# Kernel optimization log

Hardware: AMD Instinct MI355X
Metric: run time of the kernel (lower is better)

Reference implementation:

```python
import jax, jax.numpy as jnp
import numpy as np

B, S, D, F, TOPK = 8, 2048, 1024, 64, 8


def setup_inputs() -> dict:
    key = jax.random.key(0)
    ks = jax.random.split(key, 4)
    scale = 1.0 / np.sqrt(D)
    return {
        "x": jax.random.normal(ks[0], (B, S, D), dtype=jnp.float32),
        "W_top": jax.random.normal(ks[1], (D, F), dtype=jnp.float32) * scale,
        "b_top": jnp.zeros((F,), dtype=jnp.float32),
        "W_feat": jax.random.normal(ks[2], (D, F), dtype=jnp.float32) * scale,
        "b_feat": jnp.zeros((F,), dtype=jnp.float32),
        "W_gates": jax.random.normal(ks[3], (F, D), dtype=jnp.float32) * scale,
        "b_gates": jnp.zeros((F,), dtype=jnp.float32),
        "alpha": jnp.ones((1,), dtype=jnp.float32),
        "num": TOPK,
    }


def reference(x, W_top, b_top, W_feat, b_feat, W_gates, b_gates, alpha, num):
    # Router logits and top-k selection: [B,S,F] -> vals/idx [B,S,num]
    top_logits = jnp.einsum("bsd,df->bsf", x, W_top) + b_top
    vals, idx = jax.lax.top_k(top_logits, num)
    sm = jax.nn.softmax(vals, axis=-1)                     # softmax over selected experts
    # Scatter softmax'd top-k weights into dense [B,S,F] (zeros elsewhere)
    onehot = jax.nn.one_hot(idx, F, dtype=sm.dtype)        # [B,S,num,F]
    type_dense = jnp.einsum("bsk,bskf->bsf", sm, onehot)
    # Dense softmax routing branch
    feat_soft = jax.nn.softmax(jnp.einsum("bsd,df->bsf", x, W_feat) + b_feat, axis=-1)
    a = jax.nn.sigmoid(alpha)                              # [1], broadcasts
    features = a * type_dense + (1.0 - a) * feat_soft      # [B,S,F]
    # num_feature small Linear(dims,1)+Sigmoid gates fused into one GEMM
    gates = jax.nn.sigmoid(jnp.einsum("bsd,fd->bsf", x, W_gates) + b_gates)  # [B,S,F]
    # Weighted sum over feature axis; original returns shape [B,S,1]
    return jnp.sum(gates * features, axis=-1, keepdims=True)
```

## Files before the change

kernel.cpp:

```cpp
#include <hip/hip_runtime.h>
#include <hip/hip_bf16.h>
#include <math.h>

#define D_DIM 1024
#define TOKB  32
#define NCH   32

typedef short  bf16x8 __attribute__((ext_vector_type(8)));
typedef float  f32x4  __attribute__((ext_vector_type(4)));

__device__ __forceinline__ ushort f2bf(float f) {
  uint u = __float_as_uint(f);
  return (ushort)((u + 0x7fffu + ((u >> 16) & 1u)) >> 16);
}
__device__ __forceinline__ float bf2f(ushort h) {
  return __uint_as_float(((uint)h) << 16);
}
__device__ __forceinline__ float sigm(float v) {
  return 1.f / (1.f + expf(-v));
}
__device__ __forceinline__ void conv8(const f32x4 va, const f32x4 vb,
                                      bf16x8& ah, bf16x8& al) {
  uint* AH = reinterpret_cast<uint*>(&ah);
  uint* AL = reinterpret_cast<uint*>(&al);
#pragma unroll
  for (int p = 0; p < 4; ++p) {
    float a = (p < 2) ? va[2 * p]     : vb[2 * (p - 2)];
    float b = (p < 2) ? va[2 * p + 1] : vb[2 * (p - 2) + 1];
    __hip_bfloat162 h2 = __float22bfloat162_rn(float2{a, b});
    uint hu;
    __builtin_memcpy(&hu, &h2, 4);
    AH[p] = hu;
    float ra = a - __uint_as_float(hu << 16);
    float rb = b - __uint_as_float(hu & 0xffff0000u);
    __hip_bfloat162 l2 = __float22bfloat162_rn(float2{ra, rb});
    uint lu;
    __builtin_memcpy(&lu, &l2, 4);
    AL[p] = lu;
  }
}

__global__ __launch_bounds__(256) void pack_w_kernel(
    const float* __restrict__ Wt, const float* __restrict__ Wf,
    const float* __restrict__ Wg, ushort* __restrict__ Wp) {
  int gid = blockIdx.x * 256 + threadIdx.x;
  if (gid >= 32 * 12 * 64 * 4) return;
  int jp   = gid & 3;
  int t    = gid >> 2;
  int lane = t & 63;
  int t2   = t >> 6;
  int fb   = t2 % 12;
  int ks   = t2 / 12;
  int k0   = ks * 32 + ((lane >> 4) << 3) + jp * 2;
  int f    = fb * 16 + (lane & 15);
  float v0, v1;
  if (f < 64)       { v0 = Wt[k0 * 64 + f];            v1 = Wt[(k0 + 1) * 64 + f]; }
  else if (f < 128) { v0 = Wf[k0 * 64 + f - 64];       v1 = Wf[(k0 + 1) * 64 + f - 64]; }
  else              { v0 = Wg[(f - 128) * D_DIM + k0]; v1 = Wg[(f - 128) * D_DIM + k0 + 1]; }
  ushort h0 = f2bf(v0), h1 = f2bf(v1);
  ushort l0 = f2bf(v0 - bf2f(h0)), l1 = f2bf(v1 - bf2f(h1));
  size_t base = ((size_t)(ks * 12 + fb) * 2) * 512 + lane * 8 + jp * 2;
  *(uint*)(Wp + base)       = (uint)h0 | ((uint)h1 << 16);
  *(uint*)(Wp + base + 512) = (uint)l0 | ((uint)l1 << 16);
}

__global__ __launch_bounds__(512, 4) void moe_gate_kernel(
    const float* __restrict__ x, const ushort* __restrict__ Wp,
    const float* __restrict__ b_top, const float* __restrict__ b_feat,
    const float* __restrict__ b_gates, const float* __restrict__ alpha,
    const int* __restrict__ nump, float* __restrict__ out) {
  __shared__ float L[32 * 196 + 192];
  float* bsm = L + 32 * 196;
  const int tid  = threadIdx.x;
  const int lane = tid & 63;
  const int wid  = tid >> 6;
  const int tg   = wid >> 2;
  const int wc   = wid & 3;
  const int tok0 = blockIdx.x * TOKB;

  if (tid < 192)
    bsm[tid] = (tid < 64) ? b_top[tid]
             : (tid < 128) ? b_feat[tid - 64] : b_gates[tid - 128];

  const float* xp = x + (size_t)(tok0 + tg * 16 + (lane & 15)) * D_DIM
                      + ((lane >> 4) << 3);
  const ushort* wbase = Wp + (size_t)(wc * 3) * 1024 + lane * 8;

  f32x4 acc[3] = {};
  bf16x8 bAh[3], bAl[3], bBh[3], bBl[3];
  f32x4 xA[2], xB[2];

#define LOADB(BH, BL, c) do {                                        \
    const ushort* wp_ = wbase + (size_t)(c) * 12288;                 \
    _Pragma("unroll")                                                \
    for (int q = 0; q < 3; ++q) {                                    \
      BH[q] = *(const bf16x8*)(wp_ + q * 1024);                      \
      BL[q] = *(const bf16x8*)(wp_ + q * 1024 + 512);                \
    } } while (0)
#define LOADX(XR, c) do {                                            \
    XR[0] = *(const f32x4*)(xp + (c) * 32);                          \
    XR[1] = *(const f32x4*)(xp + (c) * 32 + 4); } while (0)
#define COMPUTE(XR, BH, BL) do {                                     \
    bf16x8 ah, al;                                                   \
    conv8(XR[0], XR[1], ah, al);                                     \
    _Pragma("unroll")                                                \
    for (int q = 0; q < 3; ++q) {                                    \
      acc[q] = __builtin_amdgcn_mfma_f32_16x16x32_bf16(ah, BH[q], acc[q], 0, 0, 0); \
      acc[q] = __builtin_amdgcn_mfma_f32_16x16x32_bf16(al, BH[q], acc[q], 0, 0, 0); \
      acc[q] = __builtin_amdgcn_mfma_f32_16x16x32_bf16(ah, BL[q], acc[q], 0, 0, 0); \
    } } while (0)

  LOADB(bAh, bAl, 0);
  LOADX(xA, 0);
  for (int c = 0; c < NCH; c += 2) {
    LOADB(bBh, bBl, c + 1);
    LOADX(xB, c + 1);
    COMPUTE(xA, bAh, bAl);
    if (c + 2 < NCH) {
      LOADB(bAh, bAl, c + 2);
      LOADX(xA, c + 2);
    }
    COMPUTE(xB, bBh, bBl);
  }
#undef LOADB
#undef LOADX
#undef COMPUTE

  __syncthreads();
#pragma unroll
  for (int q = 0; q < 3; ++q) {
    int f = wc * 48 + q * 16 + (lane & 15);
    int t = tg * 16 + ((lane >> 4) << 2);
    float bv = bsm[f];
#pragma unroll
    for (int r = 0; r < 4; ++r)
      L[(t + r) * 196 + f] = acc[q][r] + bv;
  }
  __syncthreads();

  if (tid < 256) {
    const int t   = tid >> 3;
    const int sub = tid & 7;
    const float* Lr = L + t * 196;
    float tp[8], ftv[8], gtv[8];
#pragma unroll
    for (int j = 0; j < 8; ++j) {
      int f = sub + 8 * j;
      tp[j]  = Lr[f];
      ftv[j] = Lr[64 + f];
      gtv[j] = sigm(Lr[128 + f]);
    }
    float mf = ftv[0];
#pragma unroll
    for (int j = 1; j < 8; ++j) mf = fmaxf(mf, ftv[j]);
#pragma unroll
    for (int m = 1; m < 8; m <<= 1) mf = fmaxf(mf, __shfl_xor(mf, m, 8));
    float Zf = 0.f, Sf = 0.f;
#pragma unroll
    for (int j = 0; j < 8; ++j) {
      float e = expf(ftv[j] - mf);
      Zf += e;
      Sf = fmaf(gtv[j], e, Sf);
    }
#pragma unroll
    for (int m = 1; m < 8; m <<= 1) {
      Zf += __shfl_xor(Zf, m, 8);
      Sf += __shfl_xor(Sf, m, 8);
    }
    int num = *nump;
    num = num < 1 ? 1 : (num > 64 ? 64 : num);
    uint sel8 = 0;
    float m0 = 0.f, Zt = 0.f, St = 0.f;
    for (int k = 0; k < num; ++k) {
      float bv = -3.4e38f; int bj = -1;
#pragma unroll
      for (int j = 0; j < 8; ++j)
        if (!((sel8 >> j) & 1u) && tp[j] > bv) { bv = tp[j]; bj = j; }
      int bf = (bj >= 0) ? (sub + 8 * bj) : (1 << 30);
#pragma unroll
      for (int m = 1; m < 8; m <<= 1) {
        float ov = __shfl_xor(bv, m, 8);
        int   of = __shfl_xor(bf, m, 8);
        if (ov > bv || (ov == bv && of < bf)) { bv = ov; bf = of; }
      }
      if (k == 0) m0 = bv;
      float e = expf(bv - m0);
      Zt += e;
      St = fmaf(sigm(Lr[128 + bf]), e, St);
      if ((bf & 7) == sub) sel8 |= 1u << (bf >> 3);
    }
    if (sub == 0) {
      float a = sigm(alpha[0]);
      out[tok0 + t] = a * (St / Zt) + (1.f - a) * (Sf / Zf);
    }
  }
}

extern "C" void kernel_launch(void* const* d_in, const int* in_sizes, int n_in,
                              void* d_out, int out_size, void* d_ws, size_t ws_size,
                              hipStream_t stream) {
  const float* x       = (const float*)d_in[0];
  const float* W_top   = (const float*)d_in[1];
  const float* b_top   = (const float*)d_in[2];
  const float* W_feat  = (const float*)d_in[3];
  const float* b_feat  = (const float*)d_in[4];
  const float* W_gates = (const float*)d_in[5];
  const float* b_gates = (const float*)d_in[6];
  const float* alpha   = (const float*)d_in[7];
  const int*   nump    = (const int*)d_in[8];
  float*       out     = (float*)d_out;
  ushort*      Wp      = (ushort*)d_ws;

  int n_tok = in_sizes[0] / D_DIM;
  hipLaunchKernelGGL(pack_w_kernel, dim3(384), dim3(256), 0, stream,
                     W_top, W_feat, W_gates, Wp);
  hipLaunchKernelGGL(moe_gate_kernel, dim3(n_tok / TOKB), dim3(512), 0, stream,
                     x, Wp, b_top, b_feat, b_gates, alpha, nump, out);
}
```

Measured before the change: 162.7 us.

## Stage packed weights into LDS via async global_load_lds double buffering

Previously every wave loaded its own copy of the packed bf16 hi/lo weight fragments straight from global memory into registers, so all 8 waves in a block fetched redundant weight data. The new code has the waves cooperatively copy each 24 KB weight chunk into shared memory with global_load_lds. It double-buffers those chunks with explicit vmcnt waits and barriers while x is still read directly into registers. This cuts global/L2 weight traffic and register pressure, but adds a block-wide barrier per chunk and raises LDS use to about 49 KB, which may limit occupancy.

```diff
diff --git a/kernel.cpp b/kernel.cpp
--- a/kernel.cpp
+++ b/kernel.cpp
@@ -18,6 +18,10 @@
 }
 __device__ __forceinline__ float sigm(float v) {
   return 1.f / (1.f + expf(-v));
+}
+__device__ __forceinline__ void gload16(const void* g, void* l) {
+  __builtin_amdgcn_global_load_lds((const __attribute__((address_space(1))) void*)g,
+                                   (__attribute__((address_space(3))) void*)l, 16, 0, 0);
 }
 __device__ __forceinline__ void conv8(const f32x4 va, const f32x4 vb,
                                       bf16x8& ah, bf16x8& al) {
@@ -69,8 +73,12 @@
     const float* __restrict__ b_top, const float* __restrict__ b_feat,
     const float* __restrict__ b_gates, const float* __restrict__ alpha,
     const int* __restrict__ nump, float* __restrict__ out) {
-  __shared__ float L[32 * 196 + 192];
-  float* bsm = L + 32 * 196;
+  __shared__ __align__(16) char smem[49920];
+  char* buf0 = smem;
+  char* buf1 = smem + 24576;
+  float* bsm = (float*)(smem + 49152);
+  float* L   = (float*)smem;
+
   const int tid  = threadIdx.x;
   const int lane = tid & 63;
   const int wid  = tid >> 6;
@@ -84,47 +92,77 @@
 
   const float* xp = x + (size_t)(tok0 + tg * 16 + (lane & 15)) * D_DIM
                       + ((lane >> 4) << 3);
-  const ushort* wbase = Wp + (size_t)(wc * 3) * 1024 + lane * 8;
+  const int stgu = wid * 1024;
+  const char* wsrc = (const char*)Wp + stgu + lane * 16;
+  const int fro = wc * 6144 + lane * 16;
 
   f32x4 acc[3] = {};
-  bf16x8 bAh[3], bAl[3], bBh[3], bBl[3];
-  f32x4 xA[2], xB[2];
-
-#define LOADB(BH, BL, c) do {                                        \
-    const ushort* wp_ = wbase + (size_t)(c) * 12288;                 \
-    _Pragma("unroll")                                                \
-    for (int q = 0; q < 3; ++q) {                                    \
-      BH[q] = *(const bf16x8*)(wp_ + q * 1024);                      \
-      BL[q] = *(const bf16x8*)(wp_ + q * 1024 + 512);                \
-    } } while (0)
-#define LOADX(XR, c) do {                                            \
-    XR[0] = *(const f32x4*)(xp + (c) * 32);                          \
-    XR[1] = *(const f32x4*)(xp + (c) * 32 + 4); } while (0)
-#define COMPUTE(XR, BH, BL) do {                                     \
+  f32x4 xA0, xA1, xB0, xB1;
+
+#define STAGE(dbuf, c) do {                                          \
+    const char* s_ = wsrc + (size_t)(c) * 24576;                     \
+    char* d_ = (dbuf) + stgu;                                        \
+    gload16(s_, d_);                                                 \
+    gload16(s_ + 8192,  d_ + 8192);                                  \
+    gload16(s_ + 16384, d_ + 16384); } while (0)
+#define COMPUTE(cbuf, X0, X1) do {                                   \
+    const char* bp_ = (cbuf) + fro;                                  \
+    bf16x8 bh0 = *(const bf16x8*)(bp_);                              \
+    bf16x8 bl0 = *(const bf16x8*)(bp_ + 1024);                       \
+    bf16x8 bh1 = *(const bf16x8*)(bp_ + 2048);                       \
+    bf16x8 bl1 = *(const bf16x8*)(bp_ + 3072);                       \
+    bf16x8 bh2 = *(const bf16x8*)(bp_ + 4096);                       \
+    bf16x8 bl2 = *(const bf16x8*)(bp_ + 5120);                       \
     bf16x8 ah, al;                                                   \
-    conv8(XR[0], XR[1], ah, al);                                     \
-    _Pragma("unroll")                                                \
-    for (int q = 0; q < 3; ++q) {                                    \
-      acc[q] = __builtin_amdgcn_mfma_f32_16x16x32_bf16(ah, BH[q], acc[q], 0, 0, 0); \
-      acc[q] = __builtin_amdgcn_mfma_f32_16x16x32_bf16(al, BH[q], acc[q], 0, 0, 0); \
-      acc[q] = __builtin_amdgcn_mfma_f32_16x16x32_bf16(ah, BL[q], acc[q], 0, 0, 0); \
-    } } while (0)
-
-  LOADB(bAh, bAl, 0);
-  LOADX(xA, 0);
-  for (int c = 0; c < NCH; c += 2) {
-    LOADB(bBh, bBl, c + 1);
-    LOADX(xB, c + 1);
-    COMPUTE(xA, bAh, bAl);
-    if (c + 2 < NCH) {
-      LOADB(bAh, bAl, c + 2);
-      LOADX(xA, c + 2);
-    }
-    COMPUTE(xB, bBh, bBl);
-  }
-#undef LOADB
-#undef LOADX
+    conv8(X0, X1, ah, al);                                           \
+    acc[0] = __builtin_amdgcn_mfma_f32_16x16x32_bf16(ah, bh0, acc[0], 0, 0, 0); \
+    acc[0] = __builtin_amdgcn_mfma_f32_16x16x32_bf16(al, bh0, acc[0], 0, 0, 0); \
+    acc[0] = __builtin_amdgcn_mfma_f32_16x16x32_bf16(ah, bl0, acc[0], 0, 0, 0); \
+    acc[1] = __builtin_amdgcn_mfma_f32_16x16x32_bf16(ah, bh1, acc[1], 0, 0, 0); \
+    acc[1] = __builtin_amdgcn_mfma_f32_16x16x32_bf16(al, bh1, acc[1], 0, 0, 0); \
+    acc[1] = __builtin_amdgcn_mfma_f32_16x16x32_bf16(ah, bl1, acc[1], 0, 0, 0); \
+    acc[2] = __builtin_amdgcn_mfma_f32_16x16x32_bf16(ah, bh2, acc[2], 0, 0, 0); \
+    acc[2] = __builtin_amdgcn_mfma_f32_16x16x32_bf16(al, bh2, acc[2], 0, 0, 0); \
+    acc[2] = __builtin_amdgcn_mfma_f32_16x16x32_bf16(ah, bl2, acc[2], 0, 0, 0); \
+  } while (0)
+#define WAITV(n) do {                                                \
+    asm volatile("s_waitcnt vmcnt(" #n ")" ::: "memory");            \
+    __builtin_amdgcn_sched_barrier(0); } while (0)
+#define BAR() do {                                                   \
+    __builtin_amdgcn_s_barrier();                                    \
+    __builtin_amdgcn_sched_barrier(0); } while (0)
+
+  STAGE(buf0, 0);
+  xA0 = *(const f32x4*)(xp);       xA1 = *(const f32x4*)(xp + 4);
+  xB0 = *(const f32x4*)(xp + 32);  xB1 = *(const f32x4*)(xp + 36);
+  WAITV(4);
+  BAR();
+
+  for (int t = 0; t < 30; t += 2) {
+    STAGE(buf1, t + 1);
+    f32x4 n0 = *(const f32x4*)(xp + (t + 2) * 32);
+    f32x4 n1 = *(const f32x4*)(xp + (t + 2) * 32 + 4);
+    COMPUTE(buf0, xA0, xA1);
+    xA0 = n0; xA1 = n1;
+    WAITV(2);
+    BAR();
+    STAGE(buf0, t + 2);
+    f32x4 m0 = *(const f32x4*)(xp + (t + 3) * 32);
+    f32x4 m1 = *(const f32x4*)(xp + (t + 3) * 32 + 4);
+    COMPUTE(buf1, xB0, xB1);
+    xB0 = m0; xB1 = m1;
+    WAITV(2);
+    BAR();
+  }
+  STAGE(buf1, 31);
+  COMPUTE(buf0, xA0, xA1);
+  WAITV(0);
+  BAR();
+  COMPUTE(buf1, xB0, xB1);
+#undef STAGE
 #undef COMPUTE
+#undef WAITV
+#undef BAR
 
   __syncthreads();
 #pragma unroll
```

After: 151.2 us. 7.1% less time.
